# Performance work log

Measured on AMD Instinct MI355X. Metric: run time of the kernel, lower is better.

## Reference

```python
import jax, jax.numpy as jnp
import numpy as np

E = 4096      # num hyperedges (events)
H1 = 512      # hidden1
H2 = 128      # hidden2 (latent)
NA, NK, NV = 8192, 4096, 1024   # nodes per type: author / keyword / venue
NNZ = 131072  # nonzeros per incidence matrix
SCALE = 0.02  # weight init scale (keeps tanh/exp in sane range)


def setup_inputs() -> dict:
    key = jax.random.key(0)
    ks = iter(jax.random.split(key, 64))
    nrm = lambda shape, s=SCALE: jax.random.normal(next(ks), shape, jnp.float32) * s
    inp = {}
    for t, N in (("a", NA), ("k", NK), ("v", NV)):
        inp["rows_" + t] = jax.random.randint(next(ks), (NNZ,), 0, N, dtype=jnp.int32)
        inp["cols_" + t] = jax.random.randint(next(ks), (NNZ,), 0, E, dtype=jnp.int32)
        inp["vals_" + t] = jax.random.uniform(next(ks), (NNZ,), jnp.float32)
        inp["Wn_" + t] = nrm((E, H1));  inp["bn_" + t] = jnp.zeros((H1,), jnp.float32)
        inp["Wzm_" + t] = nrm((H1, H2)); inp["bzm_" + t] = jnp.zeros((H2,), jnp.float32)
        inp["Wzs_" + t] = nrm((H1, H2)); inp["bzs_" + t] = jnp.zeros((H2,), jnp.float32)
        inp["We_" + t] = nrm((N, H1));  inp["be_" + t] = jnp.zeros((H1,), jnp.float32)
        inp["eps_" + t] = jax.random.normal(next(ks), (N, H2), jnp.float32)
    inp["Watt"] = nrm((H1, H1 // 2)); inp["batt"] = jnp.zeros((H1 // 2,), jnp.float32)
    inp["uatt"] = nrm((H1 // 2,), 0.1)
    inp["Wem"] = nrm((H1, H2)); inp["bem"] = jnp.zeros((H2,), jnp.float32)
    inp["Wes"] = nrm((H1, H2)); inp["bes"] = jnp.zeros((H2,), jnp.float32)
    inp["eps_e"] = jax.random.normal(next(ks), (E, H2), jnp.float32)
    return inp


def _type_branch(rows, cols, vals, N, Wn, bn, Wzm, bzm, Wzs, bzs, We, be, eps):
    # node encoder: tanh(sparse_inc @ Wn + bn);  sparse_inc is [N, E] in COO form
    h = jnp.tanh(jax.ops.segment_sum(vals[:, None] * Wn[cols], rows, num_segments=N) + bn)
    zm = h @ Wzm + bzm
    zs = h @ Wzs + bzs
    z = zm + eps * jnp.exp(zs)          # reparameterization
    # edge encoder: tanh(sparse_inc^T @ We + be) -> [E, H1]
    e = jnp.tanh(jax.ops.segment_sum(vals[:, None] * We[rows], cols, num_segments=E) + be)
    return zm, z, e


def _forward(rows_a, cols_a, vals_a, Wn_a, bn_a, Wzm_a, bzm_a, Wzs_a, bzs_a, We_a, be_a, eps_a,
             rows_k, cols_k, vals_k, Wn_k, bn_k, Wzm_k, bzm_k, Wzs_k, bzs_k, We_k, be_k, eps_k,
             rows_v, cols_v, vals_v, Wn_v, bn_v, Wzm_v, bzm_v, Wzs_v, bzs_v, We_v, be_v, eps_v,
             Watt, batt, uatt, Wem, bem, Wes, bes, eps_e):
    zm_a, z_a, e_a = _type_branch(rows_a, cols_a, vals_a, NA, Wn_a, bn_a, Wzm_a, bzm_a, Wzs_a, bzs_a, We_a, be_a, eps_a)
    zm_k, z_k, e_k = _type_branch(rows_k, cols_k, vals_k, NK, Wn_k, bn_k, Wzm_k, bzm_k, Wzs_k, bzs_k, We_k, be_k, eps_k)
    zm_v, z_v, e_v = _type_branch(rows_v, cols_v, vals_v, NV, Wn_v, bn_v, Wzm_v, bzm_v, Wzs_v, bzs_v, We_v, be_v, eps_v)

    # HyperedgeAttention over node types: [E, T=3, H1]
    edge_embeds = jnp.stack([e_a, e_k, e_v], axis=1)
    u = jnp.tanh(jnp.einsum('eth,hd->etd', edge_embeds, Watt) + batt)
    scores = jnp.einsum('etd,d->et', u, uatt)
    alphas = jax.nn.softmax(scores, axis=1)                  # [E, T]
    edge_embed = jnp.einsum('et,eth->eh', alphas, edge_embeds)  # [E, H1]

    zem = edge_embed @ Wem + bem
    zes = edge_embed @ Wes + bes
    ze = zem + eps_e * jnp.exp(zes)

    # InnerDecoder: z_node @ z_edge^T per type, flattened (sampled and mean variants)
    recon = jnp.concatenate([
        (z_a @ ze.T).ravel(), (z_k @ ze.T).ravel(), (z_v @ ze.T).ravel(),
        (zm_a @ zem.T).ravel(), (zm_k @ zem.T).ravel(), (zm_v @ zem.T).ravel(),
    ])
    return recon


def reference(rows_a, cols_a, vals_a, rows_k, cols_k, vals_k, rows_v, cols_v, vals_v,
              Wn_a, bn_a, Wzm_a, bzm_a, Wzs_a, bzs_a, We_a, be_a, eps_a,
              Wn_k, bn_k, Wzm_k, bzm_k, Wzs_k, bzs_k, We_k, be_k, eps_k,
              Wn_v, bn_v, Wzm_v, bzm_v, Wzs_v, bzs_v, We_v, be_v, eps_v,
              Watt, batt, uatt, Wem, bem, Wes, bes, eps_e):
    return _forward(rows_a, cols_a, vals_a, Wn_a, bn_a, Wzm_a, bzm_a, Wzs_a, bzs_a, We_a, be_a, eps_a,
                    rows_k, cols_k, vals_k, Wn_k, bn_k, Wzm_k, bzm_k, Wzs_k, bzs_k, We_k, be_k, eps_k,
                    rows_v, cols_v, vals_v, Wn_v, bn_v, Wzm_v, bzm_v, Wzs_v, bzs_v, We_v, be_v, eps_v,
                    Watt, batt, uatt, Wem, bem, Wes, bes, eps_e)
```

## Files before the change

kernel.cpp:

```cpp
#include <hip/hip_runtime.h>
#include <hip/hip_bf16.h>

#define NE   4096
#define D1   512
#define D2   128
#define NNZV 131072
#define MTOT 13312

typedef __attribute__((ext_vector_type(8))) short bf16x8;
typedef __attribute__((ext_vector_type(4))) float f32x4;

struct Params {
  const int*   rows[3]; const int* cols[3]; const float* vals[3];
  const float* Wn[3];  const float* bn[3];
  const float* Wzm[3]; const float* bzm[3];
  const float* Wzs[3]; const float* bzs[3];
  const float* We[3];  const float* be[3];
  const float* eps[3];
  const float* Watt; const float* batt; const float* uatt;
  const float* Wem;  const float* bem;  const float* Wes; const float* bes;
  const float* eps_e;
  int* cnt[6]; int* ptr[6]; int* cur[6]; int2* spair[6];
  __hip_bfloat16* Wbf[6];
  __hip_bfloat16* hbf[3];
  __hip_bfloat16* ebf[3];
  __hip_bfloat16* eebf;
  __hip_bfloat16* Wzmt[3];
  __hip_bfloat16* Wzst[3];
  __hip_bfloat16* Wattt;
  __hip_bfloat16* Wemt;
  __hip_bfloat16* West;
  float* scores;
  __hip_bfloat16* Zbf; __hip_bfloat16* Zmbf; __hip_bfloat16* zebf; __hip_bfloat16* zembf;
  float* out;
  int rowbase[3];
  int n8pre[7];
  int ndw;
};

__device__ __forceinline__ float bf2f(short s) {
  return __uint_as_float((unsigned)(unsigned short)s << 16);
}

__device__ __forceinline__ int nseg_of(int sub) {
  if (sub & 1) return NE;
  int t = sub >> 1;
  return t == 0 ? 8192 : (t == 1 ? 4096 : 1024);
}

__global__ void prep_kernel(Params p) {
  int i = blockIdx.x * blockDim.x + threadIdx.x;
  if (i < p.ndw) { ((int*)p.cnt[0])[i] = 0; return; }
  int c = i - p.ndw;
  if (c < p.n8pre[6]) {
    int s = 0;
#pragma unroll
    for (int k = 1; k < 6; ++k) if (c >= p.n8pre[k]) s = k;
    int off8 = c - p.n8pre[s];
    int t = s >> 1;
    const float* src = (s & 1) ? p.We[t] : p.Wn[t];
    __hip_bfloat16* dst = p.Wbf[s];
    const float4 a = *(const float4*)&src[(size_t)off8 * 8];
    const float4 b = *(const float4*)&src[(size_t)off8 * 8 + 4];
    bf16x8 o;
    o[0] = (short)__bfloat16_as_ushort(__float2bfloat16(a.x));
    o[1] = (short)__bfloat16_as_ushort(__float2bfloat16(a.y));
    o[2] = (short)__bfloat16_as_ushort(__float2bfloat16(a.z));
    o[3] = (short)__bfloat16_as_ushort(__float2bfloat16(a.w));
    o[4] = (short)__bfloat16_as_ushort(__float2bfloat16(b.x));
    o[5] = (short)__bfloat16_as_ushort(__float2bfloat16(b.y));
    o[6] = (short)__bfloat16_as_ushort(__float2bfloat16(b.z));
    o[7] = (short)__bfloat16_as_ushort(__float2bfloat16(b.w));
    *(bf16x8*)&dst[(size_t)off8 * 8] = o;
    return;
  }
  int cz = c - p.n8pre[6];
  if (cz < 6 * D1 * D2) {
    int m = cz >> 16, e = cz & 65535;
    int t = m >> 1;
    const float* src = (m & 1) ? p.Wzs[t] : p.Wzm[t];
    __hip_bfloat16* dst = (m & 1) ? p.Wzst[t] : p.Wzmt[t];
    int k = e >> 7, n = e & 127;
    dst[n * D1 + k] = __float2bfloat16(src[e]);
    return;
  }
  int cz2 = cz - 6 * D1 * D2;
  if (cz2 < D1 * 256) {
    int k = cz2 >> 8, n = cz2 & 255;
    p.Wattt[n * D1 + k] = __float2bfloat16(p.Watt[(size_t)k * 256 + n]);
    return;
  }
  int cz3 = cz2 - D1 * 256;
  if (cz3 < 2 * D1 * D2) {
    int m = cz3 >> 16, e = cz3 & 65535;
    const float* src = m ? p.Wes : p.Wem;
    __hip_bfloat16* dst = m ? p.West : p.Wemt;
    int k = e >> 7, n = e & 127;
    dst[n * D1 + k] = __float2bfloat16(src[e]);
  }
}

__global__ void hist_kernel(Params p) {
  int i = blockIdx.x * blockDim.x + threadIdx.x;
  if (i >= 6 * NNZV) return;
  int sub = i >> 17, idx = i & (NNZV - 1);
  int type = sub >> 1, dir = sub & 1;
  int seg = dir ? p.cols[type][idx] : p.rows[type][idx];
  atomicAdd(&p.cnt[sub][seg], 1);
}

__global__ __launch_bounds__(1024) void scan_kernel(Params p) {
  int sub = blockIdx.x;
  int n = nseg_of(sub);
  const int* cnt = p.cnt[sub];
  int* ptr = p.ptr[sub];
  int* cur = p.cur[sub];
  __shared__ int lds[1024];
  int tid = threadIdx.x;
  int per = (n + 1023) >> 10;
  int base = tid * per;
  int s = 0;
  for (int q = 0; q < per; ++q) { int ix = base + q; if (ix < n) s += cnt[ix]; }
  lds[tid] = s;
  __syncthreads();
  for (int off = 1; off < 1024; off <<= 1) {
    int v = (tid >= off) ? lds[tid - off] : 0;
    __syncthreads();
    lds[tid] += v;
    __syncthreads();
  }
  int prefix = (tid == 0) ? 0 : lds[tid - 1];
  for (int q = 0; q < per; ++q) {
    int ix = base + q;
    if (ix < n) { int c = cnt[ix]; ptr[ix] = prefix; cur[ix] = prefix; prefix += c; }
  }
  if (tid == 1023) ptr[n] = lds[1023];
}

__global__ void scatter_kernel(Params p) {
  int i = blockIdx.x * blockDim.x + threadIdx.x;
  if (i >= 6 * NNZV) return;
  int sub = i >> 17, idx = i & (NNZV - 1);
  int type = sub >> 1, dir = sub & 1;
  int seg = dir ? p.cols[type][idx] : p.rows[type][idx];
  int oth = dir ? p.rows[type][idx] : p.cols[type][idx];
  int pos = atomicAdd(&p.cur[sub][seg], 1);
  p.spair[sub][pos] = make_int2(oth, __float_as_int(p.vals[type][idx]));
}

__global__ __launch_bounds__(128) void spmm_kernel(Params p) {
  int g = blockIdx.x * 2 + (threadIdx.x >> 6);
  int sub, seg;
  if      (g <  8192) { sub = 0; seg = g;         }
  else if (g < 12288) { sub = 1; seg = g - 8192;  }
  else if (g < 16384) { sub = 2; seg = g - 12288; }
  else if (g < 20480) { sub = 3; seg = g - 16384; }
  else if (g < 21504) { sub = 4; seg = g - 20480; }
  else                { sub = 5; seg = g - 21504; }
  int type = sub >> 1, dir = sub & 1;
  const __hip_bfloat16* W = p.Wbf[sub];
  const float* bias = dir ? p.be[type] : p.bn[type];
  const int*  ptr  = p.ptr[sub];
  const int2* pair = p.spair[sub];
  int lane = threadIdx.x & 63;
  int c0 = lane * 8;
  float acc[8];
#pragma unroll
  for (int j = 0; j < 8; ++j) acc[j] = 0.f;
  int q0 = ptr[seg], q1 = ptr[seg + 1];
  int q = q0;
  for (; q + 4 <= q1; q += 4) {
    int2 pr0 = pair[q], pr1 = pair[q + 1], pr2 = pair[q + 2], pr3 = pair[q + 3];
    const bf16x8 w0 = *(const bf16x8*)(W + (size_t)pr0.x * D1 + c0);
    const bf16x8 w1 = *(const bf16x8*)(W + (size_t)pr1.x * D1 + c0);
    const bf16x8 w2 = *(const bf16x8*)(W + (size_t)pr2.x * D1 + c0);
    const bf16x8 w3 = *(const bf16x8*)(W + (size_t)pr3.x * D1 + c0);
    float v0 = __int_as_float(pr0.y), v1 = __int_as_float(pr1.y);
    float v2 = __int_as_float(pr2.y), v3 = __int_as_float(pr3.y);
#pragma unroll
    for (int j = 0; j < 8; ++j)
      acc[j] += v0 * bf2f(w0[j]) + v1 * bf2f(w1[j]) + v2 * bf2f(w2[j]) + v3 * bf2f(w3[j]);
  }
  for (; q < q1; ++q) {
    int2 pr = pair[q];
    const bf16x8 wv = *(const bf16x8*)(W + (size_t)pr.x * D1 + c0);
    float v = __int_as_float(pr.y);
#pragma unroll
    for (int j = 0; j < 8; ++j) acc[j] += v * bf2f(wv[j]);
  }
  const float4 b0 = *(const float4*)&bias[c0];
  const float4 b1 = *(const float4*)&bias[c0 + 4];
  float r[8];
  r[0] = tanhf(acc[0] + b0.x); r[1] = tanhf(acc[1] + b0.y);
  r[2] = tanhf(acc[2] + b0.z); r[3] = tanhf(acc[3] + b0.w);
  r[4] = tanhf(acc[4] + b1.x); r[5] = tanhf(acc[5] + b1.y);
  r[6] = tanhf(acc[6] + b1.z); r[7] = tanhf(acc[7] + b1.w);
  bf16x8 ob;
#pragma unroll
  for (int j = 0; j < 8; ++j) ob[j] = (short)__bfloat16_as_ushort(__float2bfloat16(r[j]));
  __hip_bfloat16* outp = dir ? p.ebf[type] : p.hbf[type];
  *(bf16x8*)&outp[(size_t)seg * D1 + c0] = ob;
}

__global__ __launch_bounds__(128) void zmzs_kernel(Params p) {
  int b = blockIdx.x;
  int type, blk;
  if      (b < 256) { type = 0; blk = b;       }
  else if (b < 384) { type = 1; blk = b - 256; }
  else              { type = 2; blk = b - 384; }
  int row0 = blk * 32;
  const __hip_bfloat16* A  = p.hbf[type];
  const __hip_bfloat16* Bm = p.Wzmt[type];
  const __hip_bfloat16* Bs = p.Wzst[type];
  int wid = threadIdx.x >> 6, lane = threadIdx.x & 63;
  int rloc = lane & 15, kg = lane >> 4;
  int mrow = row0 + wid * 16 + rloc;
  f32x4 accm[8], accs[8];
  f32x4 zero = {0.f, 0.f, 0.f, 0.f};
#pragma unroll
  for (int nf = 0; nf < 8; ++nf) { accm[nf] = zero; accs[nf] = zero; }
  for (int kk = 0; kk < 16; ++kk) {
    bf16x8 a = *(const bf16x8*)(A + (size_t)mrow * D1 + kk * 32 + kg * 8);
#pragma unroll
    for (int nf = 0; nf < 8; ++nf) {
      int ncol = nf * 16 + rloc;
      bf16x8 bm = *(const bf16x8*)(Bm + (size_t)ncol * D1 + kk * 32 + kg * 8);
      accm[nf] = __builtin_amdgcn_mfma_f32_16x16x32_bf16(a, bm, accm[nf], 0, 0, 0);
      bf16x8 bs = *(const bf16x8*)(Bs + (size_t)ncol * D1 + kk * 32 + kg * 8);
      accs[nf] = __builtin_amdgcn_mfma_f32_16x16x32_bf16(a, bs, accs[nf], 0, 0, 0);
    }
  }
  int base = p.rowbase[type];
  const float* eps = p.eps[type];
  const float* bzm = p.bzm[type];
  const float* bzs = p.bzs[type];
  int rbase = row0 + wid * 16 + kg * 4;
#pragma unroll
  for (int nf = 0; nf < 8; ++nf) {
    int col = nf * 16 + rloc;
    float bm = bzm[col], bs = bzs[col];
#pragma unroll
    for (int jj = 0; jj < 4; ++jj) {
      int row = rbase + jj;
      float zm = accm[nf][jj] + bm;
      float zs = accs[nf][jj] + bs;
      float ep = eps[(size_t)row * D2 + col];
      float z  = zm + ep * expf(zs);
      size_t oi = (size_t)(base + row) * D2 + col;
      p.Zmbf[oi] = __float2bfloat16(zm);
      p.Zbf[oi]  = __float2bfloat16(z);
    }
  }
}

__global__ __launch_bounds__(256) void scores_kernel(Params p) {
  int wtile = blockIdx.x * 4 + (threadIdx.x >> 6);
  int t = wtile >> 8;
  int tile = wtile & 255;
  const __hip_bfloat16* A = p.ebf[t];
  const __hip_bfloat16* B = p.Wattt;
  int lane = threadIdx.x & 63;
  int rloc = lane & 15, kg = lane >> 4;
  int mrow = tile * 16 + rloc;
  f32x4 acc[16];
  f32x4 zero = {0.f, 0.f, 0.f, 0.f};
#pragma unroll
  for (int nf = 0; nf < 16; ++nf) acc[nf] = zero;
  for (int kk = 0; kk < 16; ++kk) {
    bf16x8 a = *(const bf16x8*)(A + (size_t)mrow * D1 + kk * 32 + kg * 8);
#pragma unroll
    for (int nf = 0; nf < 16; ++nf) {
      int ncol = nf * 16 + rloc;
      bf16x8 bv = *(const bf16x8*)(B + (size_t)ncol * D1 + kk * 32 + kg * 8);
      acc[nf] = __builtin_amdgcn_mfma_f32_16x16x32_bf16(a, bv, acc[nf], 0, 0, 0);
    }
  }
  float part[4] = {0.f, 0.f, 0.f, 0.f};
#pragma unroll
  for (int nf = 0; nf < 16; ++nf) {
    int col = nf * 16 + rloc;
    float ua = p.uatt[col], ba = p.batt[col];
#pragma unroll
    for (int jj = 0; jj < 4; ++jj)
      part[jj] += ua * tanhf(acc[nf][jj] + ba);
  }
#pragma unroll
  for (int off = 1; off < 16; off <<= 1) {
#pragma unroll
    for (int jj = 0; jj < 4; ++jj)
      part[jj] += __shfl_xor(part[jj], off, 64);
  }
  if (rloc == 0) {
#pragma unroll
    for (int jj = 0; jj < 4; ++jj) {
      int e = tile * 16 + kg * 4 + jj;
      p.scores[e * 3 + t] = part[jj];
    }
  }
}

__global__ __launch_bounds__(256) void combine_kernel(Params p) {
  int e = blockIdx.x * 4 + (threadIdx.x >> 6);
  int lane = threadIdx.x & 63;
  float s0 = p.scores[e * 3 + 0];
  float s1 = p.scores[e * 3 + 1];
  float s2 = p.scores[e * 3 + 2];
  float m = fmaxf(s0, fmaxf(s1, s2));
  float a0 = expf(s0 - m), a1 = expf(s1 - m), a2 = expf(s2 - m);
  float inv = 1.f / (a0 + a1 + a2);
  a0 *= inv; a1 *= inv; a2 *= inv;
  int c0 = lane * 8;
  const bf16x8 va = *(const bf16x8*)(p.ebf[0] + (size_t)e * D1 + c0);
  const bf16x8 vk = *(const bf16x8*)(p.ebf[1] + (size_t)e * D1 + c0);
  const bf16x8 vv = *(const bf16x8*)(p.ebf[2] + (size_t)e * D1 + c0);
  bf16x8 o;
#pragma unroll
  for (int j = 0; j < 8; ++j) {
    float v = a0 * bf2f(va[j]) + a1 * bf2f(vk[j]) + a2 * bf2f(vv[j]);
    o[j] = (short)__bfloat16_as_ushort(__float2bfloat16(v));
  }
  *(bf16x8*)&p.eebf[(size_t)e * D1 + c0] = o;
}

__global__ __launch_bounds__(128) void zemzs_kernel(Params p) {
  int row0 = blockIdx.x * 32;
  const __hip_bfloat16* A  = p.eebf;
  const __hip_bfloat16* Bm = p.Wemt;
  const __hip_bfloat16* Bs = p.West;
  int wid = threadIdx.x >> 6, lane = threadIdx.x & 63;
  int rloc = lane & 15, kg = lane >> 4;
  int mrow = row0 + wid * 16 + rloc;
  f32x4 accm[8], accs[8];
  f32x4 zero = {0.f, 0.f, 0.f, 0.f};
#pragma unroll
  for (int nf = 0; nf < 8; ++nf) { accm[nf] = zero; accs[nf] = zero; }
  for (int kk = 0; kk < 16; ++kk) {
    bf16x8 a = *(const bf16x8*)(A + (size_t)mrow * D1 + kk * 32 + kg * 8);
#pragma unroll
    for (int nf = 0; nf < 8; ++nf) {
      int ncol = nf * 16 + rloc;
      bf16x8 bm = *(const bf16x8*)(Bm + (size_t)ncol * D1 + kk * 32 + kg * 8);
      accm[nf] = __builtin_amdgcn_mfma_f32_16x16x32_bf16(a, bm, accm[nf], 0, 0, 0);
      bf16x8 bs = *(const bf16x8*)(Bs + (size_t)ncol * D1 + kk * 32 + kg * 8);
      accs[nf] = __builtin_amdgcn_mfma_f32_16x16x32_bf16(a, bs, accs[nf], 0, 0, 0);
    }
  }
  const float* bem = p.bem;
  const float* bes = p.bes;
  int rbase = row0 + wid * 16 + kg * 4;
#pragma unroll
  for (int nf = 0; nf < 8; ++nf) {
    int col = nf * 16 + rloc;
    float bm = bem[col], bs = bes[col];
#pragma unroll
    for (int jj = 0; jj < 4; ++jj) {
      int row = rbase + jj;
      float zm = accm[nf][jj] + bm;
      float zs = accs[nf][jj] + bs;
      float ep = p.eps_e[(size_t)row * D2 + col];
      float z  = zm + ep * expf(zs);
      size_t oi = (size_t)row * D2 + col;
      p.zembf[oi] = __float2bfloat16(zm);
      p.zebf[oi]  = __float2bfloat16(z);
    }
  }
}

#define DT_N 128
__global__ __launch_bounds__(256) void decode_kernel(Params p) {
  __shared__ __align__(16) float cs[64][DT_N + 4];
  int which = blockIdx.z;
  const __hip_bfloat16* A = which ? p.Zmbf  : p.Zbf;
  const __hip_bfloat16* B = which ? p.zembf : p.zebf;
  float* C = p.out + (size_t)which * MTOT * NE;
  int n0 = blockIdx.x * DT_N;
  int m0 = blockIdx.y * 64;
  int wid  = threadIdx.x >> 6;
  int lane = threadIdx.x & 63;
  int rloc = lane & 15;
  int kg   = lane >> 4;
  int mrow = m0 + wid * 16 + rloc;
  bf16x8 a[4];
#pragma unroll
  for (int kk = 0; kk < 4; ++kk)
    a[kk] = *(const bf16x8*)(A + (size_t)mrow * D2 + kk * 32 + kg * 8);
  f32x4 acc[DT_N / 16];
  f32x4 zero = {0.f, 0.f, 0.f, 0.f};
#pragma unroll
  for (int nf = 0; nf < DT_N / 16; ++nf) acc[nf] = zero;
#pragma unroll
  for (int nf = 0; nf < DT_N / 16; ++nf) {
    int ncol = n0 + nf * 16 + rloc;
#pragma unroll
    for (int kk = 0; kk < 4; ++kk) {
      bf16x8 bv = *(const bf16x8*)(B + (size_t)ncol * D2 + kk * 32 + kg * 8);
      acc[nf] = __builtin_amdgcn_mfma_f32_16x16x32_bf16(a[kk], bv, acc[nf], 0, 0, 0);
    }
  }
#pragma unroll
  for (int nf = 0; nf < DT_N / 16; ++nf)
#pragma unroll
    for (int jj = 0; jj < 4; ++jj)
      cs[wid * 16 + kg * 4 + jj][nf * 16 + rloc] = acc[nf][jj];
  __syncthreads();
  int r_l  = threadIdx.x >> 5;
  int c4   = (threadIdx.x & 31) * 4;
#pragma unroll
  for (int it = 0; it < 8; ++it) {
    int r = it * 8 + r_l;
    f32x4 v = *(const f32x4*)&cs[r][c4];
    __builtin_nontemporal_store(v, (f32x4*)&C[(size_t)(m0 + r) * NE + n0 + c4]);
  }
}

extern "C" void kernel_launch(void* const* d_in, const int* in_sizes, int n_in,
                              void* d_out, int out_size, void* d_ws, size_t ws_size,
                              hipStream_t stream) {
  (void)in_sizes; (void)n_in; (void)out_size; (void)ws_size;
  static const int Ns[3] = {8192, 4096, 1024};
  static const int NsegH[6] = {8192, 4096, 4096, 4096, 1024, 4096};

  Params p;
  for (int t = 0; t < 3; ++t) {
    const int o = t * 12;
    p.rows[t] = (const int*)d_in[o + 0];
    p.cols[t] = (const int*)d_in[o + 1];
    p.vals[t] = (const float*)d_in[o + 2];
    p.Wn[t]   = (const float*)d_in[o + 3];
    p.bn[t]   = (const float*)d_in[o + 4];
    p.Wzm[t]  = (const float*)d_in[o + 5];
    p.bzm[t]  = (const float*)d_in[o + 6];
    p.Wzs[t]  = (const float*)d_in[o + 7];
    p.bzs[t]  = (const float*)d_in[o + 8];
    p.We[t]   = (const float*)d_in[o + 9];
    p.be[t]   = (const float*)d_in[o + 10];
    p.eps[t]  = (const float*)d_in[o + 11];
  }
  p.Watt  = (const float*)d_in[36];
  p.batt  = (const float*)d_in[37];
  p.uatt  = (const float*)d_in[38];
  p.Wem   = (const float*)d_in[39];
  p.bem   = (const float*)d_in[40];
  p.Wes   = (const float*)d_in[41];
  p.bes   = (const float*)d_in[42];
  p.eps_e = (const float*)d_in[43];
  p.out = (float*)d_out;
  p.rowbase[0] = 0; p.rowbase[1] = 8192; p.rowbase[2] = 12288;

  char* ws = (char*)d_ws;
  size_t off = 0;
  auto alloc = [&](size_t bytes) -> char* {
    char* r = ws + off;
    off += (bytes + 255) & ~(size_t)255;
    return r;
  };
  for (int s = 0; s < 6; ++s) p.cnt[s] = (int*)alloc((size_t)(NsegH[s] + 1) * 4);
  size_t cnt_bytes = off;
  for (int s = 0; s < 6; ++s) {
    p.ptr[s]   = (int*)alloc((size_t)(NsegH[s] + 1) * 4);
    p.cur[s]   = (int*)alloc((size_t)(NsegH[s] + 1) * 4);
    p.spair[s] = (int2*)alloc((size_t)NNZV * 8);
  }
  for (int s = 0; s < 6; ++s) {
    int t = s >> 1;
    int nrows = (s & 1) ? Ns[t] : NE;
    p.Wbf[s] = (__hip_bfloat16*)alloc((size_t)nrows * D1 * 2);
  }
  for (int t = 0; t < 3; ++t) p.hbf[t]  = (__hip_bfloat16*)alloc((size_t)Ns[t] * D1 * 2);
  for (int t = 0; t < 3; ++t) p.ebf[t]  = (__hip_bfloat16*)alloc((size_t)NE * D1 * 2);
  p.eebf = (__hip_bfloat16*)alloc((size_t)NE * D1 * 2);
  for (int t = 0; t < 3; ++t) p.Wzmt[t] = (__hip_bfloat16*)alloc((size_t)D2 * D1 * 2);
  for (int t = 0; t < 3; ++t) p.Wzst[t] = (__hip_bfloat16*)alloc((size_t)D2 * D1 * 2);
  p.Wattt = (__hip_bfloat16*)alloc((size_t)256 * D1 * 2);
  p.Wemt  = (__hip_bfloat16*)alloc((size_t)D2 * D1 * 2);
  p.West  = (__hip_bfloat16*)alloc((size_t)D2 * D1 * 2);
  p.scores = (float*)alloc((size_t)NE * 3 * 4);
  p.Zbf    = (__hip_bfloat16*)alloc((size_t)MTOT * D2 * 2);
  p.Zmbf   = (__hip_bfloat16*)alloc((size_t)MTOT * D2 * 2);
  p.zebf   = (__hip_bfloat16*)alloc((size_t)NE * D2 * 2);
  p.zembf  = (__hip_bfloat16*)alloc((size_t)NE * D2 * 2);

  p.ndw = (int)(cnt_bytes >> 2);
  p.n8pre[0] = 0;
  for (int s = 0; s < 6; ++s) {
    int t = s >> 1;
    int nrows = (s & 1) ? Ns[t] : NE;
    p.n8pre[s + 1] = p.n8pre[s] + nrows * (D1 / 8);
  }

  int prep_threads = p.ndw + p.n8pre[6] + 6 * D1 * D2 + D1 * 256 + 2 * D1 * D2;
  prep_kernel    <<<(prep_threads + 255) / 256, 256, 0, stream>>>(p);
  hist_kernel    <<<(6 * NNZV + 255) / 256, 256, 0, stream>>>(p);
  scan_kernel    <<<6, 1024, 0, stream>>>(p);
  scatter_kernel <<<(6 * NNZV + 255) / 256, 256, 0, stream>>>(p);
  spmm_kernel    <<<12800, 128, 0, stream>>>(p);
  zmzs_kernel    <<<416, 128, 0, stream>>>(p);
  scores_kernel  <<<192, 256, 0, stream>>>(p);
  combine_kernel <<<1024, 256, 0, stream>>>(p);
  zemzs_kernel   <<<128, 128, 0, stream>>>(p);
  decode_kernel  <<<dim3(NE / DT_N, 208, 2), 256, 0, stream>>>(p);
}
```

Measured before the change: 556.6 us.

## Retile decode GEMM to 16x1024 tiles with full-row contiguous stores

The decode kernel now makes each block own 16 output rows by 1024 columns instead of 64 by 128. All four waves share one A fragment and each covers 256 columns, so every store instruction writes a 4KB contiguous row segment. The store also switches from nontemporal to a normal cached store. The change aims to improve write coalescing for the roughly 436 MB output, at the cost of more B reloads per block, 64 accumulator registers per thread and 64KB of LDS per block, which limits occupancy.

```diff
diff --git a/kernel.cpp b/kernel.cpp
--- a/kernel.cpp
+++ b/kernel.cpp
@@ -366,31 +366,30 @@
   }
 }
 
-#define DT_N 128
 __global__ __launch_bounds__(256) void decode_kernel(Params p) {
-  __shared__ __align__(16) float cs[64][DT_N + 4];
+  __shared__ __align__(16) float cs[16][1024];
   int which = blockIdx.z;
   const __hip_bfloat16* A = which ? p.Zmbf  : p.Zbf;
   const __hip_bfloat16* B = which ? p.zembf : p.zebf;
   float* C = p.out + (size_t)which * MTOT * NE;
-  int n0 = blockIdx.x * DT_N;
-  int m0 = blockIdx.y * 64;
+  int m0 = blockIdx.x * 16;
+  int n0 = blockIdx.y * 1024;
   int wid  = threadIdx.x >> 6;
   int lane = threadIdx.x & 63;
   int rloc = lane & 15;
   int kg   = lane >> 4;
-  int mrow = m0 + wid * 16 + rloc;
+  int mrow = m0 + rloc;
   bf16x8 a[4];
 #pragma unroll
   for (int kk = 0; kk < 4; ++kk)
     a[kk] = *(const bf16x8*)(A + (size_t)mrow * D2 + kk * 32 + kg * 8);
-  f32x4 acc[DT_N / 16];
+  f32x4 acc[16];
   f32x4 zero = {0.f, 0.f, 0.f, 0.f};
 #pragma unroll
-  for (int nf = 0; nf < DT_N / 16; ++nf) acc[nf] = zero;
-#pragma unroll
-  for (int nf = 0; nf < DT_N / 16; ++nf) {
-    int ncol = n0 + nf * 16 + rloc;
+  for (int nf = 0; nf < 16; ++nf) acc[nf] = zero;
+#pragma unroll
+  for (int nf = 0; nf < 16; ++nf) {
+    int ncol = n0 + wid * 256 + nf * 16 + rloc;
 #pragma unroll
     for (int kk = 0; kk < 4; ++kk) {
       bf16x8 bv = *(const bf16x8*)(B + (size_t)ncol * D2 + kk * 32 + kg * 8);
@@ -398,18 +397,15 @@
     }
   }
 #pragma unroll
-  for (int nf = 0; nf < DT_N / 16; ++nf)
+  for (int nf = 0; nf < 16; ++nf)
 #pragma unroll
     for (int jj = 0; jj < 4; ++jj)
-      cs[wid * 16 + kg * 4 + jj][nf * 16 + rloc] = acc[nf][jj];
+      cs[kg * 4 + jj][wid * 256 + nf * 16 + rloc] = acc[nf][jj];
   __syncthreads();
-  int r_l  = threadIdx.x >> 5;
-  int c4   = (threadIdx.x & 31) * 4;
-#pragma unroll
-  for (int it = 0; it < 8; ++it) {
-    int r = it * 8 + r_l;
-    f32x4 v = *(const f32x4*)&cs[r][c4];
-    __builtin_nontemporal_store(v, (f32x4*)&C[(size_t)(m0 + r) * NE + n0 + c4]);
+#pragma unroll
+  for (int r = 0; r < 16; ++r) {
+    f32x4 v = *(const f32x4*)&cs[r][threadIdx.x * 4];
+    *(f32x4*)&C[(size_t)(m0 + r) * NE + n0 + threadIdx.x * 4] = v;
   }
 }
 
@@ -498,5 +494,5 @@
   scores_kernel  <<<192, 256, 0, stream>>>(p);
   combine_kernel <<<1024, 256, 0, stream>>>(p);
   zemzs_kernel   <<<128, 128, 0, stream>>>(p);
-  decode_kernel  <<<dim3(NE / DT_N, 208, 2), 256, 0, stream>>>(p);
-}
+  decode_kernel  <<<dim3(MTOT / 16, 4, 2), 256, 0, stream>>>(p);
+}
```

Result: slower. 572.3 us (+2.8%).
